# Kernel optimization log

Hardware: AMD Instinct MI355X
Metric: run time of the kernel (lower is better)

The kernel has to match this reference:

```python
import jax, jax.numpy as jnp
import numpy as np

# geomloss SamplesLoss defaults for loss='sinkhorn'
BLUR = 0.05
SCALING = 0.5
P = 1  # norm=1 -> cost C(x,y) = ||x - y||_2


def _cost(x, y):
    # Euclidean distance cost (p=1). x:(B,N,D), y:(B,M,D) -> (B,N,M)
    d2 = (jnp.sum(x * x, -1)[:, :, None]
          - 2.0 * jnp.einsum('bnd,bmd->bnm', x, y)
          + jnp.sum(y * y, -1)[:, None, :])
    return jnp.sqrt(jnp.clip(d2, 1e-12, None))  # tiny clamp keeps sqrt grad finite on diagonal


def _softmin(eps, C, h):
    # f_i = -eps * logsumexp_j( h_j - C_ij / eps );  C:(B,N,M), h:(B,M) -> (B,N)
    return -eps * jax.nn.logsumexp(h[:, None, :] - C / eps, axis=2)


def _eps_schedule(diameter):
    # geomloss epsilon_schedule(p, diameter, blur, scaling)
    return ([diameter ** P]
            + [float(np.exp(e)) for e in np.arange(P * np.log(diameter), P * np.log(BLUR), P * np.log(SCALING))]
            + [BLUR ** P])


def _sinkhorn_divergence(x, y):
    # Debiased Sinkhorn divergence (geomloss, tensorized backend, balanced OT).
    B, N, D = x.shape
    M = y.shape[1]
    a_log = jnp.full((B, N), -np.log(N), dtype=x.dtype)  # uniform weights (log)
    b_log = jnp.full((B, M), -np.log(M), dtype=x.dtype)

    C_xy = _cost(x, y)
    C_yx = jnp.swapaxes(C_xy, 1, 2)  # symmetric cost
    C_xx = _cost(x, x)
    C_yy = _cost(y, y)

    # diameter of the joint point cloud (geomloss max_diameter); concrete python float
    xf = np.asarray(x).reshape(-1, D)
    yf = np.asarray(y).reshape(-1, D)
    mins = np.minimum(xf.min(0), yf.min(0))
    maxs = np.maximum(xf.max(0), yf.max(0))
    diameter = float(np.linalg.norm(maxs - mins))
    eps_list = _eps_schedule(diameter)

    sg = jax.lax.stop_gradient

    # initialization at the largest eps
    eps = eps_list[0]
    f_aa = _softmin(eps, C_xx, a_log)
    g_bb = _softmin(eps, C_yy, b_log)
    g_ab = _softmin(eps, C_yx, a_log)
    f_ba = _softmin(eps, C_xy, b_log)

    # epsilon-annealing loop with symmetric (averaged) updates; no grad flows
    # through this loop (outputs are stop_gradient'ed in the final extrapolation)
    for eps in eps_list:
        ft_ba = _softmin(eps, C_xy, b_log + g_ab / eps)
        gt_ab = _softmin(eps, C_yx, a_log + f_ba / eps)
        f_ba = 0.5 * (f_ba + ft_ba)
        g_ab = 0.5 * (g_ab + gt_ab)
        ft_aa = _softmin(eps, C_xx, a_log + f_aa / eps)
        gt_bb = _softmin(eps, C_yy, b_log + g_bb / eps)
        f_aa = 0.5 * (f_aa + ft_aa)
        g_bb = 0.5 * (g_bb + gt_bb)

    # last extrapolation at eps = blur^p with detached dual potentials (envelope theorem)
    eps = eps_list[-1]
    f_ba_new = _softmin(eps, C_xy, sg(b_log + g_ab / eps))
    g_ab_new = _softmin(eps, C_yx, sg(a_log + f_ba / eps))
    f_aa = _softmin(eps, C_xx, sg(a_log + f_aa / eps))
    g_bb = _softmin(eps, C_yy, sg(b_log + g_bb / eps))
    f_ba, g_ab = f_ba_new, g_ab_new

    a = jnp.exp(a_log)
    b = jnp.exp(b_log)
    # S_eps(a,b) = <a, f_ba - f_aa> + <b, g_ab - g_bb>, per batch element
    return jnp.sum(a * (f_ba - f_aa), -1) + jnp.sum(b * (g_ab - g_bb), -1)


def setup_inputs() -> dict:
    key = jax.random.key(0)
    k1, k2 = jax.random.split(key)
    pre = jax.random.normal(k1, (2, 4096, 2), dtype=jnp.float32)
    gt = jax.random.normal(k2, (2, 4096, 2), dtype=jnp.float32)
    return {"pre": pre, "gt": gt}


def reference(pre, gt):
    return _sinkhorn_divergence(pre, gt).mean()
```

## Files before the change

kernel.cpp:

```cpp
#include <hip/hip_runtime.h>
#include <math.h>

#define NPTS 4096
#define NB 2
#define K_TOTAL 12
#define BLOCK 256
#define TILE 128
#define NT (NPTS / TILE)

#define SCHED_OFF 0
#define MBUF_OFF 32
#define P_OFF 64
#define POT_SZ (4 * NB * NPTS)
#define PART_OFF (P_OFF + POT_SZ)

#if __has_builtin(__builtin_amdgcn_exp2f)
#define EXP2F __builtin_amdgcn_exp2f
#else
#define EXP2F exp2f
#endif
#if __has_builtin(__builtin_amdgcn_logf)
#define LOG2F __builtin_amdgcn_logf
#else
#define LOG2F log2f
#endif
#if __has_builtin(__builtin_amdgcn_sqrtf)
#define FSQRTF __builtin_amdgcn_sqrtf
#else
#define FSQRTF sqrtf
#endif

#define BASE_LOGW -8.31776616671934f
#define LOG2E 1.4426950408889634f
#define LN2 0.69314718055994531f

typedef float v2f __attribute__((ext_vector_type(2)));

__device__ __forceinline__ unsigned encf(float f) {
  unsigned u = __float_as_uint(f);
  return (u & 0x80000000u) ? ~u : (u | 0x80000000u);
}
__device__ __forceinline__ float decf(unsigned k) {
  return __uint_as_float((k & 0x80000000u) ? (k ^ 0x80000000u) : ~k);
}

__global__ __launch_bounds__(BLOCK) void k_init(
    const float2* __restrict__ x, const float2* __restrict__ y, float* ws)
{
  const int tid = threadIdx.x;
  const int bid = blockIdx.x;

  if (bid > 0) {
    for (int i = (bid - 1) * BLOCK + tid; i < POT_SZ; i += 63 * BLOCK)
      ws[P_OFF + i] = 0.0f;
    return;
  }

  if (tid < 8) {
    unsigned* MB = (unsigned*)ws + MBUF_OFF;
    MB[8 + tid] = encf(BASE_LOGW);
    MB[tid] = encf(-1e30f);
  }

  float mnx = 1e30f, mny = 1e30f, mxx = -1e30f, mxy = -1e30f;
  for (int i = tid; i < NB * NPTS; i += BLOCK) {
    float2 p = x[i];
    mnx = fminf(mnx, p.x); mxx = fmaxf(mxx, p.x);
    mny = fminf(mny, p.y); mxy = fmaxf(mxy, p.y);
    float2 q = y[i];
    mnx = fminf(mnx, q.x); mxx = fmaxf(mxx, q.x);
    mny = fminf(mny, q.y); mxy = fmaxf(mxy, q.y);
  }
  for (int o = 32; o; o >>= 1) {
    mnx = fminf(mnx, __shfl_xor(mnx, o, 64));
    mxx = fmaxf(mxx, __shfl_xor(mxx, o, 64));
    mny = fminf(mny, __shfl_xor(mny, o, 64));
    mxy = fmaxf(mxy, __shfl_xor(mxy, o, 64));
  }
  __shared__ float r[4][4];
  const int wave = tid >> 6, lane = tid & 63;
  if (lane == 0) { r[0][wave] = mnx; r[1][wave] = mxx; r[2][wave] = mny; r[3][wave] = mxy; }
  __syncthreads();
  if (tid == 0) {
    mnx = fminf(fminf(r[0][0], r[0][1]), fminf(r[0][2], r[0][3]));
    mxx = fmaxf(fmaxf(r[1][0], r[1][1]), fmaxf(r[1][2], r[1][3]));
    mny = fminf(fminf(r[2][0], r[2][1]), fminf(r[2][2], r[2][3]));
    mxy = fmaxf(fmaxf(r[3][0], r[3][1]), fmaxf(r[3][2], r[3][3]));
    float rx = mxx - mnx, ry = mxy - mny;
    float dia = sqrtf(rx * rx + ry * ry);

    double a = log((double)dia);
    double stop = log(0.05);
    double stp = log(0.5);
    int cnt = (int)ceil((stop - a) / stp);
    if (cnt < 0) cnt = 0;
    if (cnt > K_TOTAL - 4) cnt = K_TOTAL - 4;

    float* sch = ws + SCHED_OFF;
    sch[0] = dia; sch[1] = 0.0f;
    sch[2] = dia; sch[3] = 0.5f;
    for (int k = 0; k < cnt; k++) {
      sch[2 * (2 + k)] = (float)exp(a + (double)k * stp);
      sch[2 * (2 + k) + 1] = 0.5f;
    }
    sch[2 * (2 + cnt)] = 0.05f; sch[2 * (2 + cnt) + 1] = 0.5f;
    for (int s = 3 + cnt; s < K_TOTAL - 1; s++) { sch[2 * s] = 0.05f; sch[2 * s + 1] = 1.0f; }
    sch[2 * (K_TOTAL - 1)] = 0.05f; sch[2 * (K_TOTAL - 1) + 1] = 0.0f;
  }
}

__global__ __launch_bounds__(BLOCK, 4) void k_tiles(
    const float2* __restrict__ xpts, const float2* __restrict__ ypts,
    float* __restrict__ ws, int stepi)
{
  __shared__ float rXs[TILE], rYs[TILE], rVs[TILE];
  __shared__ float cXs[144], cYs[144], cVs[144];
  __shared__ float tPart[16][129];

  const int tid = threadIdx.x;
  const int id = blockIdx.x;

  const float2* rowp; const float2* colp;
  const float* prow; const float* pcol;
  int ti, tj, pbr, pbc;
  bool dual;

  if (id < NB * NT * NT) {
    const int b = id >> 10;
    const int t = id & (NT * NT - 1);
    ti = t >> 5; tj = t & (NT - 1);
    rowp = xpts + b * NPTS; colp = ypts + b * NPTS;
    prow = ws + P_OFF + (0 * NB + b) * NPTS;
    pcol = ws + P_OFF + (1 * NB + b) * NPTS;
    pbr = 0 * NB + b; pbc = 1 * NB + b;
    dual = true;
  } else {
    const int id2 = id - NB * NT * NT;
    const int mat = id2 >> 11;
    const int t2 = id2 & 2047;
    const int b = t2 >> 10;
    const int t = t2 & 1023;
    ti = t >> 5; tj = t & 31;
    if (ti > tj) return;
    const float2* pts = mat ? ypts : xpts;
    rowp = pts + b * NPTS; colp = rowp;
    const int p = 2 + mat;
    prow = ws + P_OFF + (p * NB + b) * NPTS; pcol = prow;
    pbr = p * NB + b; pbc = pbr;
    dual = (ti != tj);
  }

  const float eps = ws[SCHED_OFF + 2 * stepi];
  const float sc = LOG2E / eps;
  const float inv_eps = 1.0f / eps;
  const unsigned* MB = (const unsigned*)ws + MBUF_OFF + 8 * ((stepi + 1) & 1);

  if (id == 0 && tid < 8)
    ((unsigned*)ws)[MBUF_OFF + 8 * (stepi & 1) + tid] = encf(-1e30f);

  if (tid < TILE) {
    const int r = ti * TILE + tid;
    float2 pr = rowp[r];
    float h = fmaf(prow[r], inv_eps, BASE_LOGW);
    rXs[tid] = pr.x * sc; rYs[tid] = pr.y * sc;
    rVs[tid] = EXP2F((h - decf(MB[pbr])) * LOG2E);
  } else {
    const int k = tid - TILE;
    const int r = tj * TILE + k;
    float2 pc = colp[r];
    float h = fmaf(pcol[r], inv_eps, BASE_LOGW);
    const int kk = k + (k >> 3);
    cXs[kk] = pc.x * sc; cYs[kk] = pc.y * sc;
    cVs[kk] = EXP2F((h - decf(MB[pbc])) * LOG2E);
  }
  __syncthreads();

  const int tx = tid & 15, ty = tid >> 4;
  float rx[8], ry[8], rv[8];
  v2f cx2[4], cy2[4], cv2[4], racc2[8], cacc2[4];
#pragma unroll
  for (int q = 0; q < 8; q++) {
    rx[q] = rXs[ty * 8 + q]; ry[q] = rYs[ty * 8 + q]; rv[q] = rVs[ty * 8 + q];
    racc2[q] = (v2f){0.0f, 0.0f};
  }
#pragma unroll
  for (int j = 0; j < 4; j++) {
    const int ci = tx * 9 + 2 * j;
    cx2[j] = (v2f){cXs[ci], cXs[ci + 1]};
    cy2[j] = (v2f){cYs[ci], cYs[ci + 1]};
    cv2[j] = (v2f){cVs[ci], cVs[ci + 1]};
    cacc2[j] = (v2f){0.0f, 0.0f};
  }

#pragma unroll
  for (int q = 0; q < 8; q++) {
    const v2f rxq = (v2f){rx[q], rx[q]};
    const v2f ryq = (v2f){ry[q], ry[q]};
    const v2f rvq = (v2f){rv[q], rv[q]};
#pragma unroll
    for (int j = 0; j < 4; j++) {
      v2f dx = rxq - cx2[j];
      v2f dy = ryq - cy2[j];
      v2f d2 = dx * dx + dy * dy;
      float t0 = FSQRTF(d2.x), t1 = FSQRTF(d2.y);
      v2f K = (v2f){EXP2F(-t0), EXP2F(-t1)};
      racc2[q] += K * cv2[j];
      cacc2[j] += K * rvq;
    }
  }

  float* part = ws + PART_OFF;

#pragma unroll
  for (int q = 0; q < 8; q++) tPart[tx][ty * 8 + q] = racc2[q].x + racc2[q].y;
  __syncthreads();
  if (tid < TILE) {
    float s = 0.0f;
#pragma unroll
    for (int t = 0; t < 16; t++) s += tPart[t][tid];
    part[(pbr * NT + tj) * NPTS + ti * TILE + tid] = s;
  }
  __syncthreads();

#pragma unroll
  for (int j = 0; j < 4; j++) {
    tPart[ty][tx * 8 + 2 * j] = cacc2[j].x;
    tPart[ty][tx * 8 + 2 * j + 1] = cacc2[j].y;
  }
  __syncthreads();
  if (dual && tid < TILE) {
    float s = 0.0f;
#pragma unroll
    for (int t = 0; t < 16; t++) s += tPart[t][tid];
    part[(pbc * NT + ti) * NPTS + tj * TILE + tid] = s;
  }
}

__global__ __launch_bounds__(BLOCK) void k_combine(float* __restrict__ ws, int stepi)
{
  const int bid = blockIdx.x;
  const int pb = bid >> 4, chunk = bid & 15;
  const int tid = threadIdx.x;

  const float eps = ws[SCHED_OFF + 2 * stepi];
  const float w = ws[SCHED_OFF + 2 * stepi + 1];
  int ni = stepi + 1; if (ni > K_TOTAL - 1) ni = K_TOTAL - 1;
  const float inv_eps_n = 1.0f / ws[SCHED_OFF + 2 * ni];
  unsigned* MB = (unsigned*)ws + MBUF_OFF;
  const float Mh = decf(MB[8 * ((stepi + 1) & 1) + pb]);

  const int r = chunk * BLOCK + tid;
  const float* pp = ws + PART_OFF + pb * NT * NPTS + r;
  float s = 0.0f;
#pragma unroll
  for (int c = 0; c < NT; c++) s += pp[c * NPTS];

  float* Pp = ws + P_OFF + pb * NPTS;
  s = fmaxf(s, 1e-37f);
  float ft = -eps * fmaf(LN2, LOG2F(s), Mh);
  float fo = Pp[r];
  float fn = (w >= 1.0f) ? fo : fmaf(w, fo, (1.0f - w) * ft);
  Pp[r] = fn;
  float lmax = fmaf(fn, inv_eps_n, BASE_LOGW);

  for (int o = 32; o; o >>= 1) lmax = fmaxf(lmax, __shfl_xor(lmax, o, 64));
  __shared__ float red[4];
  if ((tid & 63) == 0) red[tid >> 6] = lmax;
  __syncthreads();
  if (tid == 0) {
    float M = fmaxf(fmaxf(red[0], red[1]), fmaxf(red[2], red[3]));
    atomicMax(&MB[8 * (stepi & 1) + pb], encf(M));
  }
}

__global__ __launch_bounds__(1024) void k_reduce(
    const float* __restrict__ pot, float* __restrict__ out)
{
  const int tid = threadIdx.x;
  double acc = 0.0;
  for (int i = tid; i < POT_SZ; i += 1024) {
    double v = (double)pot[i];
    acc += (i < 2 * NB * NPTS) ? v : -v;
  }
  for (int o = 32; o; o >>= 1) acc += __shfl_xor(acc, o, 64);
  __shared__ double rd[16];
  const int wave = tid >> 6, lane = tid & 63;
  if (lane == 0) rd[wave] = acc;
  __syncthreads();
  if (tid == 0) {
    double s = 0.0;
#pragma unroll
    for (int i = 0; i < 16; i++) s += rd[i];
    out[0] = (float)(s / (double)(NB * NPTS));
  }
}

extern "C" void kernel_launch(void* const* d_in, const int* in_sizes, int n_in,
                              void* d_out, int out_size, void* d_ws, size_t ws_size,
                              hipStream_t stream)
{
  const float2* x = (const float2*)d_in[0];
  const float2* y = (const float2*)d_in[1];
  float* ws = (float*)d_ws;

  k_init<<<64, BLOCK, 0, stream>>>(x, y, ws);

  const int nblocks = NB * NT * NT + 2 * NB * NT * NT;
  for (int s = 0; s < K_TOTAL; s++) {
    k_tiles<<<nblocks, BLOCK, 0, stream>>>(x, y, ws, s);
    k_combine<<<128, BLOCK, 0, stream>>>(ws, s);
  }
  k_reduce<<<1, 1024, 0, stream>>>(ws + P_OFF, (float*)d_out);
}
```

Baseline: 445.6 us.

## Fuse combine into tile kernel with per-tile local max stabilization

Removes the separate combine kernel. Each tile block now recomputes its own row and column potentials from the previous step's partial sums, using double-buffered partials and potentials, and rescales per-tile local maxima instead of a global atomicMax. The symmetric-matrix grid is also compacted to launch only upper-triangle tiles instead of returning early from lower ones, and the final reduce finishes the last potentials. This halves the number of launches and drops the atomics, but every tile block redundantly reads 32 partial columns for its rows and columns, which costs more memory traffic per block.

Measured after the change: 455.3 us. 1.02x slower.

```diff
diff --git a/kernel.cpp b/kernel.cpp
--- a/kernel.cpp
+++ b/kernel.cpp
@@ -9,10 +9,11 @@
 #define NT (NPTS / TILE)
 
 #define SCHED_OFF 0
-#define MBUF_OFF 32
-#define P_OFF 64
+#define ML_OFF 32
+#define P_OFF 576
 #define POT_SZ (4 * NB * NPTS)
-#define PART_OFF (P_OFF + POT_SZ)
+#define PART_OFF (P_OFF + 2 * POT_SZ)
+#define PART_SZ (4 * NB * NT * NPTS)
 
 #if __has_builtin(__builtin_amdgcn_exp2f)
 #define EXP2F __builtin_amdgcn_exp2f
@@ -36,14 +37,6 @@
 
 typedef float v2f __attribute__((ext_vector_type(2)));
 
-__device__ __forceinline__ unsigned encf(float f) {
-  unsigned u = __float_as_uint(f);
-  return (u & 0x80000000u) ? ~u : (u | 0x80000000u);
-}
-__device__ __forceinline__ float decf(unsigned k) {
-  return __uint_as_float((k & 0x80000000u) ? (k ^ 0x80000000u) : ~k);
-}
-
 __global__ __launch_bounds__(BLOCK) void k_init(
     const float2* __restrict__ x, const float2* __restrict__ y, float* ws)
 {
@@ -51,15 +44,9 @@
   const int bid = blockIdx.x;
 
   if (bid > 0) {
-    for (int i = (bid - 1) * BLOCK + tid; i < POT_SZ; i += 63 * BLOCK)
+    for (int i = (bid - 1) * BLOCK + tid; i < 2 * POT_SZ; i += 63 * BLOCK)
       ws[P_OFF + i] = 0.0f;
     return;
-  }
-
-  if (tid < 8) {
-    unsigned* MB = (unsigned*)ws + MBUF_OFF;
-    MB[8 + tid] = encf(BASE_LOGW);
-    MB[tid] = encf(-1e30f);
   }
 
   float mnx = 1e30f, mny = 1e30f, mxx = -1e30f, mxy = -1e30f;
@@ -116,12 +103,14 @@
   __shared__ float rXs[TILE], rYs[TILE], rVs[TILE];
   __shared__ float cXs[144], cYs[144], cVs[144];
   __shared__ float tPart[16][129];
+  __shared__ float sfb[2][32];
+  __shared__ float smx[2];
+  __shared__ float wmax[4];
 
   const int tid = threadIdx.x;
   const int id = blockIdx.x;
 
   const float2* rowp; const float2* colp;
-  const float* prow; const float* pcol;
   int ti, tj, pbr, pbc;
   bool dual;
 
@@ -130,49 +119,85 @@
     const int t = id & (NT * NT - 1);
     ti = t >> 5; tj = t & (NT - 1);
     rowp = xpts + b * NPTS; colp = ypts + b * NPTS;
-    prow = ws + P_OFF + (0 * NB + b) * NPTS;
-    pcol = ws + P_OFF + (1 * NB + b) * NPTS;
     pbr = 0 * NB + b; pbc = 1 * NB + b;
     dual = true;
   } else {
     const int id2 = id - NB * NT * NT;
-    const int mat = id2 >> 11;
-    const int t2 = id2 & 2047;
-    const int b = t2 >> 10;
-    const int t = t2 & 1023;
-    ti = t >> 5; tj = t & 31;
-    if (ti > tj) return;
+    const int mat = id2 / 1056;
+    const int rem = id2 - mat * 1056;
+    const int b = rem / 528;
+    const int k = rem - b * 528;
+    int t0 = (int)((65.0f - FSQRTF((float)(4225 - 8 * k))) * 0.5f);
+    while (t0 * (65 - t0) / 2 > k) t0--;
+    while ((t0 + 1) * (64 - t0) / 2 <= k) t0++;
+    ti = t0; tj = t0 + (k - t0 * (65 - t0) / 2);
     const float2* pts = mat ? ypts : xpts;
     rowp = pts + b * NPTS; colp = rowp;
-    const int p = 2 + mat;
-    prow = ws + P_OFF + (p * NB + b) * NPTS; pcol = prow;
-    pbr = p * NB + b; pbc = pbr;
+    pbr = (2 + mat) * NB + b; pbc = pbr;
     dual = (ti != tj);
   }
 
   const float eps = ws[SCHED_OFF + 2 * stepi];
   const float sc = LOG2E / eps;
   const float inv_eps = 1.0f / eps;
-  const unsigned* MB = (const unsigned*)ws + MBUF_OFF + 8 * ((stepi + 1) & 1);
-
-  if (id == 0 && tid < 8)
-    ((unsigned*)ws)[MBUF_OFF + 8 * (stepi & 1) + tid] = encf(-1e30f);
-
-  if (tid < TILE) {
-    const int r = ti * TILE + tid;
-    float2 pr = rowp[r];
-    float h = fmaf(prow[r], inv_eps, BASE_LOGW);
-    rXs[tid] = pr.x * sc; rYs[tid] = pr.y * sc;
-    rVs[tid] = EXP2F((h - decf(MB[pbr])) * LOG2E);
+  const int ppar = (stepi - 1) & 1;
+  const int cpar = stepi & 1;
+
+  if (stepi > 0 && tid < 64) {
+    const int c = tid & 31, side = tid >> 5;
+    const int pb_own = side ? pbc : pbr;
+    const int spb = (pb_own < 4) ? (pb_own ^ 2) : pb_own;
+    float ml = ws[ML_OFF + ppar * 256 + spb * NT + c];
+    float mm = ml;
+    mm = fmaxf(mm, __shfl_xor(mm, 1, 64));
+    mm = fmaxf(mm, __shfl_xor(mm, 2, 64));
+    mm = fmaxf(mm, __shfl_xor(mm, 4, 64));
+    mm = fmaxf(mm, __shfl_xor(mm, 8, 64));
+    mm = fmaxf(mm, __shfl_xor(mm, 16, 64));
+    sfb[side][c] = EXP2F((ml - mm) * LOG2E);
+    if (c == 0) smx[side] = mm;
+  }
+  __syncthreads();
+
+  const int side = tid >> 7, kk0 = tid & 127;
+  const int pb_own = side ? pbc : pbr;
+  const int tile_own = side ? tj : ti;
+  const int r = tile_own * TILE + kk0;
+  float2 pt = (side ? colp : rowp)[r];
+
+  float h;
+  if (stepi == 0) {
+    h = BASE_LOGW;
   } else {
-    const int k = tid - TILE;
-    const int r = tj * TILE + k;
-    float2 pc = colp[r];
-    float h = fmaf(pcol[r], inv_eps, BASE_LOGW);
-    const int kk = k + (k >> 3);
-    cXs[kk] = pc.x * sc; cYs[kk] = pc.y * sc;
-    cVs[kk] = EXP2F((h - decf(MB[pbc])) * LOG2E);
-  }
+    const float eps_p = ws[SCHED_OFF + 2 * (stepi - 1)];
+    const float w_p = ws[SCHED_OFF + 2 * (stepi - 1) + 1];
+    const float* pprev = ws + PART_OFF + ppar * PART_SZ + (pb_own * NT) * NPTS + r;
+    float s = 0.0f;
+#pragma unroll
+    for (int c = 0; c < NT; c++) s += pprev[c * NPTS] * sfb[side][c];
+    s = fmaxf(s, 1e-37f);
+    float ft = -eps_p * fmaf(LN2, LOG2F(s), smx[side]);
+    float po = ws[P_OFF + cpar * POT_SZ + pb_own * NPTS + r];
+    float pn = (w_p >= 1.0f) ? po : fmaf(w_p, po, (1.0f - w_p) * ft);
+    ws[P_OFF + ppar * POT_SZ + pb_own * NPTS + r] = pn;
+    h = fmaf(pn, inv_eps, BASE_LOGW);
+  }
+
+  float hm = h;
+  for (int o = 32; o; o >>= 1) hm = fmaxf(hm, __shfl_xor(hm, o, 64));
+  if ((tid & 63) == 0) wmax[tid >> 6] = hm;
+  __syncthreads();
+  const float Mloc = fmaxf(wmax[2 * side], wmax[2 * side + 1]);
+
+  if (side == 0) {
+    rXs[kk0] = pt.x * sc; rYs[kk0] = pt.y * sc;
+    rVs[kk0] = EXP2F((h - Mloc) * LOG2E);
+  } else {
+    const int kk = kk0 + (kk0 >> 3);
+    cXs[kk] = pt.x * sc; cYs[kk] = pt.y * sc;
+    cVs[kk] = EXP2F((h - Mloc) * LOG2E);
+  }
+  if (kk0 == 0) ws[ML_OFF + cpar * 256 + pb_own * NT + tile_own] = Mloc;
   __syncthreads();
 
   const int tx = tid & 15, ty = tid >> 4;
@@ -209,7 +234,7 @@
     }
   }
 
-  float* part = ws + PART_OFF;
+  float* part = ws + PART_OFF + cpar * PART_SZ;
 
 #pragma unroll
   for (int q = 0; q < 8; q++) tPart[tx][ty * 8 + q] = racc2[q].x + racc2[q].y;
@@ -236,51 +261,41 @@
   }
 }
 
-__global__ __launch_bounds__(BLOCK) void k_combine(float* __restrict__ ws, int stepi)
+__global__ __launch_bounds__(1024) void k_reduce(const float* __restrict__ ws_c,
+                                                 float* __restrict__ out)
 {
-  const int bid = blockIdx.x;
-  const int pb = bid >> 4, chunk = bid & 15;
+  const float* ws = ws_c;
   const int tid = threadIdx.x;
-
-  const float eps = ws[SCHED_OFF + 2 * stepi];
-  const float w = ws[SCHED_OFF + 2 * stepi + 1];
-  int ni = stepi + 1; if (ni > K_TOTAL - 1) ni = K_TOTAL - 1;
-  const float inv_eps_n = 1.0f / ws[SCHED_OFF + 2 * ni];
-  unsigned* MB = (unsigned*)ws + MBUF_OFF;
-  const float Mh = decf(MB[8 * ((stepi + 1) & 1) + pb]);
-
-  const int r = chunk * BLOCK + tid;
-  const float* pp = ws + PART_OFF + pb * NT * NPTS + r;
-  float s = 0.0f;
-#pragma unroll
-  for (int c = 0; c < NT; c++) s += pp[c * NPTS];
-
-  float* Pp = ws + P_OFF + pb * NPTS;
-  s = fmaxf(s, 1e-37f);
-  float ft = -eps * fmaf(LN2, LOG2F(s), Mh);
-  float fo = Pp[r];
-  float fn = (w >= 1.0f) ? fo : fmaf(w, fo, (1.0f - w) * ft);
-  Pp[r] = fn;
-  float lmax = fmaf(fn, inv_eps_n, BASE_LOGW);
-
-  for (int o = 32; o; o >>= 1) lmax = fmaxf(lmax, __shfl_xor(lmax, o, 64));
-  __shared__ float red[4];
-  if ((tid & 63) == 0) red[tid >> 6] = lmax;
-  __syncthreads();
-  if (tid == 0) {
-    float M = fmaxf(fmaxf(red[0], red[1]), fmaxf(red[2], red[3]));
-    atomicMax(&MB[8 * (stepi & 1) + pb], encf(M));
-  }
-}
-
-__global__ __launch_bounds__(1024) void k_reduce(
-    const float* __restrict__ pot, float* __restrict__ out)
-{
-  const int tid = threadIdx.x;
+  const int lpar = (K_TOTAL - 1) & 1;
+  const float eps_l = ws[SCHED_OFF + 2 * (K_TOTAL - 1)];
+
+  __shared__ float sfl[8][32];
+  __shared__ float mm8[8];
+  if (tid < 256) {
+    const int g = tid >> 5, c = tid & 31;
+    const int spb = (g < 4) ? (g ^ 2) : g;
+    float ml = ws[ML_OFF + lpar * 256 + spb * NT + c];
+    float mm = ml;
+    mm = fmaxf(mm, __shfl_xor(mm, 1, 64));
+    mm = fmaxf(mm, __shfl_xor(mm, 2, 64));
+    mm = fmaxf(mm, __shfl_xor(mm, 4, 64));
+    mm = fmaxf(mm, __shfl_xor(mm, 8, 64));
+    mm = fmaxf(mm, __shfl_xor(mm, 16, 64));
+    sfl[g][c] = EXP2F((ml - mm) * LOG2E);
+    if (c == 0) mm8[g] = mm;
+  }
+  __syncthreads();
+
   double acc = 0.0;
-  for (int i = tid; i < POT_SZ; i += 1024) {
-    double v = (double)pot[i];
-    acc += (i < 2 * NB * NPTS) ? v : -v;
+  for (int idx = tid; idx < 4 * NB * NPTS; idx += 1024) {
+    const int pb = idx >> 12, r = idx & (NPTS - 1);
+    const float* pp = ws + PART_OFF + lpar * PART_SZ + (pb * NT) * NPTS + r;
+    float s = 0.0f;
+#pragma unroll
+    for (int c = 0; c < NT; c++) s += pp[c * NPTS] * sfl[pb][c];
+    s = fmaxf(s, 1e-37f);
+    float f = -eps_l * fmaf(LN2, LOG2F(s), mm8[pb]);
+    acc += (pb < 2 * NB) ? (double)f : -(double)f;
   }
   for (int o = 32; o; o >>= 1) acc += __shfl_xor(acc, o, 64);
   __shared__ double rd[16];
@@ -305,10 +320,9 @@
 
   k_init<<<64, BLOCK, 0, stream>>>(x, y, ws);
 
-  const int nblocks = NB * NT * NT + 2 * NB * NT * NT;
+  const int nblocks = NB * NT * NT + 2 * NB * (NT * (NT + 1)) / 2;
   for (int s = 0; s < K_TOTAL; s++) {
     k_tiles<<<nblocks, BLOCK, 0, stream>>>(x, y, ws, s);
-    k_combine<<<128, BLOCK, 0, stream>>>(ws, s);
-  }
-  k_reduce<<<1, 1024, 0, stream>>>(ws + P_OFF, (float*)d_out);
+  }
+  k_reduce<<<1, 1024, 0, stream>>>(ws, (float*)d_out);
 }
```
